# Optimization experiments

Measured on AMD Instinct MI355X. Metric: run time of the kernel, lower is better.

Reference implementation:

```python
import jax, jax.numpy as jnp
import numpy as np

B, N, D = 256, 131072, 256
TEMP = 0.05
EPS_SM = 1e-6
EPS_LOG = 1e-6
NUM_CLUSTERS = 1000


def _l2norm(x):
    return x / jnp.linalg.norm(x, axis=-1, keepdims=True)


def setup_inputs() -> dict:
    key = jax.random.key(0)
    k1, k2, k3, k4, k5 = jax.random.split(key, 5)
    # re-ID features are L2-normalized in practice; keeps exp(logits/temp) finite
    inputs = _l2norm(jax.random.normal(k1, (B, D), jnp.float32))
    indexes = jax.random.randint(k2, (B,), 0, N)
    labels = jax.random.randint(k3, (N,), 0, NUM_CLUSTERS)  # pseudo cluster ids buffer
    cluster_features = _l2norm(jax.random.normal(k4, (N, D), jnp.float32))
    instance_features = _l2norm(jax.random.normal(k5, (N, D), jnp.float32))
    return {
        "inputs": inputs,
        "cluster_features": cluster_features,
        "instance_features": instance_features,
        "indexes": indexes,
        "labels": labels,
    }


def reference(inputs, cluster_features, instance_features, indexes, labels):
    # targets = labels[indexes]
    targets = labels[indexes]
    # bank similarity GEMM, temperature scaling
    logits = jnp.matmul(inputs, cluster_features.T) / TEMP  # [B, N]
    # module's custom softmax: exp / (sum + eps)  (intentionally no max-subtract)
    exps = jnp.exp(logits)
    masked_sim = exps / (jnp.sum(exps, axis=1, keepdims=True) + EPS_SM)
    logp = jnp.log(masked_sim + EPS_LOG)
    # F.nll_loss: mean of -logp at target column
    loss = -jnp.mean(jnp.take_along_axis(logp, targets[:, None], axis=1))
    return loss
```

## Files before the change

kernel.cpp:

```cpp
#include <hip/hip_runtime.h>
#include <hip/hip_bf16.h>
#include <cstdint>

#define B_ 256
#define N_ 131072
#define D_ 256
#define INV_TEMP 20.0f
#define EPS_SM 1e-6f
#define EPS_LOG 1e-6f

#define TPB 512
#define BN 128
#define BK 64
#define TILES 4
#define LDB 72
#define BUFE (BN * LDB)
#define NSLOT 32

typedef __bf16 bf16_t;
typedef bf16_t bf16x8 __attribute__((ext_vector_type(8)));
typedef float f32x4 __attribute__((ext_vector_type(4)));

__device__ inline ushort f2bf(float f) {
  uint32_t u = __builtin_bit_cast(uint32_t, f);
  u += 0x7FFFu + ((u >> 16) & 1u);
  return (ushort)(u >> 16);
}

__global__ __launch_bounds__(TPB, 2)
void gemm_rowsum(const float* __restrict__ inp, const float* __restrict__ cf,
                 float* __restrict__ rowsum) {
  __shared__ ushort smem[2 * BUFE];
  const int tid  = threadIdx.x;
  const int wave = tid >> 6;
  const int lane = tid & 63;
  const int m15  = lane & 15;
  const int q    = lane >> 4;

  bf16x8 areg[8][2];
#pragma unroll
  for (int kc = 0; kc < 4; ++kc) {
    const int row = tid >> 1, half = tid & 1;
    const float* src = inp + row * D_ + kc * BK + half * 32;
#pragma unroll
    for (int i = 0; i < 8; ++i) {
      const float4 v = *(const float4*)(src + i * 4);
      ushort4 w = {f2bf(v.x), f2bf(v.y), f2bf(v.z), f2bf(v.w)};
      *(ushort4*)(&smem[row * LDB + half * 32 + i * 4]) = w;
    }
    __syncthreads();
#pragma unroll
    for (int mb = 0; mb < 2; ++mb)
#pragma unroll
      for (int ks = 0; ks < 2; ++ks)
        areg[kc * 2 + ks][mb] = __builtin_bit_cast(
            bf16x8, *(const uint4*)(&smem[(wave * 32 + mb * 16 + m15) * LDB + ks * 32 + q * 8]));
    __syncthreads();
  }

  const size_t nbase = (size_t)blockIdx.x * (TILES * BN);
  const int brow = tid >> 2, bcg = tid & 3;

  f32x4 acc[2][8];
  float rs[2][4];
#pragma unroll
  for (int mb = 0; mb < 2; ++mb) {
#pragma unroll
    for (int nb = 0; nb < 8; ++nb) acc[mb][nb] = (f32x4){0.f, 0.f, 0.f, 0.f};
#pragma unroll
    for (int r = 0; r < 4; ++r) rs[mb][r] = 0.f;
  }

  float4 ldbuf[2][4];
#define LDADDR(c) (cf + (nbase + (size_t)((c) >> 2) * BN + brow) * D_ + ((c) & 3) * BK + bcg * 16)

#pragma unroll
  for (int i = 0; i < 4; ++i) ldbuf[0][i] = *(const float4*)(LDADDR(0) + i * 4);
#pragma unroll
  for (int i = 0; i < 4; ++i) ldbuf[1][i] = *(const float4*)(LDADDR(1) + i * 4);
  {
    ushort* dst = &smem[0 * BUFE + brow * LDB + bcg * 16];
#pragma unroll
    for (int i = 0; i < 4; ++i) {
      const float4 v = ldbuf[0][i];
      ushort4 w = {f2bf(v.x), f2bf(v.y), f2bf(v.z), f2bf(v.w)};
      *(ushort4*)(dst + i * 4) = w;
    }
  }

#pragma unroll
  for (int c = 0; c < TILES * 4; ++c) {
    __syncthreads();
    if (c + 2 < TILES * 4) {
#pragma unroll
      for (int i = 0; i < 4; ++i) ldbuf[c & 1][i] = *(const float4*)(LDADDR(c + 2) + i * 4);
    }
    const ushort* bs = &smem[(c & 1) * BUFE];
#pragma unroll
    for (int ks = 0; ks < 2; ++ks) {
      bf16x8 bfr[8];
#pragma unroll
      for (int nb = 0; nb < 8; ++nb)
        bfr[nb] = __builtin_bit_cast(
            bf16x8, *(const uint4*)(&bs[(nb * 16 + m15) * LDB + ks * 32 + q * 8]));
#pragma unroll
      for (int mb = 0; mb < 2; ++mb)
#pragma unroll
        for (int nb = 0; nb < 8; ++nb)
          acc[mb][nb] = __builtin_amdgcn_mfma_f32_16x16x32_bf16(
              areg[(c & 3) * 2 + ks][mb], bfr[nb], acc[mb][nb], 0, 0, 0);
    }
    if ((c & 3) == 3) {
#pragma unroll
      for (int mb = 0; mb < 2; ++mb)
#pragma unroll
        for (int nb = 0; nb < 8; ++nb)
#pragma unroll
          for (int r = 0; r < 4; ++r)
            rs[mb][r] += __expf(acc[mb][nb][r] * INV_TEMP);
      if (c + 1 < TILES * 4) {
#pragma unroll
        for (int mb = 0; mb < 2; ++mb)
#pragma unroll
          for (int nb = 0; nb < 8; ++nb) acc[mb][nb] = (f32x4){0.f, 0.f, 0.f, 0.f};
      }
    }
    if (c + 1 < TILES * 4) {
      ushort* dst = &smem[((c + 1) & 1) * BUFE + brow * LDB + bcg * 16];
#pragma unroll
      for (int i = 0; i < 4; ++i) {
        const float4 v = ldbuf[(c + 1) & 1][i];
        ushort4 w = {f2bf(v.x), f2bf(v.y), f2bf(v.z), f2bf(v.w)};
        *(ushort4*)(dst + i * 4) = w;
      }
    }
  }

#pragma unroll
  for (int off = 8; off >= 1; off >>= 1)
#pragma unroll
    for (int mb = 0; mb < 2; ++mb)
#pragma unroll
      for (int r = 0; r < 4; ++r)
        rs[mb][r] += __shfl_xor(rs[mb][r], off, 64);

  if (m15 == 0) {
    float* slot = rowsum + (blockIdx.x & (NSLOT - 1)) * B_;
#pragma unroll
    for (int mb = 0; mb < 2; ++mb)
#pragma unroll
      for (int r = 0; r < 4; ++r)
        atomicAdd(&slot[wave * 32 + mb * 16 + q * 4 + r], rs[mb][r]);
  }
#undef LDADDR
}

__global__ __launch_bounds__(1024)
void finalize_loss(const float* __restrict__ inp, const float* __restrict__ cf,
                   const int* __restrict__ idx, const int* __restrict__ lab,
                   const float* __restrict__ rowsum, float* __restrict__ out) {
  __shared__ float red[1024];
  __shared__ float lg[256];
  const int tid = threadIdx.x;
  const int b = tid >> 2, part = tid & 3;
  const int t = lab[idx[b]];
  const float4* a = (const float4*)(inp + b * D_ + part * 64);
  const float4* c = (const float4*)(cf + (size_t)t * D_ + part * 64);
  float dot = 0.f;
#pragma unroll
  for (int i = 0; i < 16; ++i) {
    const float4 x = a[i], y = c[i];
    dot += x.x * y.x + x.y * y.y + x.z * y.z + x.w * y.w;
  }
  red[tid] = dot;
  __syncthreads();
  if (tid < 256) {
    const float d = red[tid * 4] + red[tid * 4 + 1] + red[tid * 4 + 2] + red[tid * 4 + 3];
    float S = 0.f;
#pragma unroll
    for (int s = 0; s < NSLOT; ++s) S += rowsum[s * B_ + tid];
    lg[tid] = __logf(__expf(d * INV_TEMP) / (S + EPS_SM) + EPS_LOG);
  }
  __syncthreads();
  for (int off = 128; off >= 1; off >>= 1) {
    if (tid < off) lg[tid] += lg[tid + off];
    __syncthreads();
  }
  if (tid == 0) out[0] = -lg[0] * (1.0f / 256.0f);
}

extern "C" void kernel_launch(void* const* d_in, const int* in_sizes, int n_in,
                              void* d_out, int out_size, void* d_ws, size_t ws_size,
                              hipStream_t stream) {
  const float* inp = (const float*)d_in[0];
  const float* cf  = (const float*)d_in[1];
  const int* idx = (const int*)d_in[3];
  const int* lab = (const int*)d_in[4];
  float* out = (float*)d_out;
  float* rowsum = (float*)d_ws;

  hipMemsetAsync(rowsum, 0, NSLOT * B_ * sizeof(float), stream);
  gemm_rowsum<<<dim3(N_ / (TILES * BN)), dim3(TPB), 0, stream>>>(inp, cf, rowsum);
  finalize_loss<<<dim3(1), dim3(1024), 0, stream>>>(inp, cf, idx, lab, rowsum, out);
}
```

Before: 287.8 us.

## Replace atomic rowsum slots with per-block partials and lighter LDS barrier

After: 290.8 us. No clear change (+1.1%).

```diff
diff --git a/kernel.cpp b/kernel.cpp
--- a/kernel.cpp
+++ b/kernel.cpp
@@ -13,9 +13,9 @@
 #define BN 128
 #define BK 64
 #define TILES 4
+#define NBLK (N_ / (TILES * BN))
 #define LDB 72
 #define BUFE (BN * LDB)
-#define NSLOT 32
 
 typedef __bf16 bf16_t;
 typedef bf16_t bf16x8 __attribute__((ext_vector_type(8)));
@@ -25,6 +25,10 @@
   uint32_t u = __builtin_bit_cast(uint32_t, f);
   u += 0x7FFFu + ((u >> 16) & 1u);
   return (ushort)(u >> 16);
+}
+
+__device__ inline void lds_barrier() {
+  asm volatile("s_waitcnt lgkmcnt(0)\n\ts_barrier" ::: "memory");
 }
 
 __global__ __launch_bounds__(TPB, 2)
@@ -90,7 +94,7 @@
 
 #pragma unroll
   for (int c = 0; c < TILES * 4; ++c) {
-    __syncthreads();
+    lds_barrier();
     if (c + 2 < TILES * 4) {
 #pragma unroll
       for (int i = 0; i < 4; ++i) ldbuf[c & 1][i] = *(const float4*)(LDADDR(c + 2) + i * 4);
@@ -145,12 +149,12 @@
         rs[mb][r] += __shfl_xor(rs[mb][r], off, 64);
 
   if (m15 == 0) {
-    float* slot = rowsum + (blockIdx.x & (NSLOT - 1)) * B_;
+    float* slot = rowsum + (size_t)blockIdx.x * B_;
 #pragma unroll
     for (int mb = 0; mb < 2; ++mb)
 #pragma unroll
       for (int r = 0; r < 4; ++r)
-        atomicAdd(&slot[wave * 32 + mb * 16 + q * 4 + r], rs[mb][r]);
+        slot[wave * 32 + mb * 16 + q * 4 + r] = rs[mb][r];
   }
 #undef LDADDR
 }
@@ -162,10 +166,11 @@
   __shared__ float red[1024];
   __shared__ float lg[256];
   const int tid = threadIdx.x;
-  const int b = tid >> 2, part = tid & 3;
-  const int t = lab[idx[b]];
-  const float4* a = (const float4*)(inp + b * D_ + part * 64);
-  const float4* c = (const float4*)(cf + (size_t)t * D_ + part * 64);
+  const int r = tid & 255, p = tid >> 8;
+
+  const int t = lab[idx[r]];
+  const float4* a = (const float4*)(inp + r * D_ + p * 64);
+  const float4* c = (const float4*)(cf + (size_t)t * D_ + p * 64);
   float dot = 0.f;
 #pragma unroll
   for (int i = 0; i < 16; ++i) {
@@ -173,13 +178,18 @@
     dot += x.x * y.x + x.y * y.y + x.z * y.z + x.w * y.w;
   }
   red[tid] = dot;
+
+  float S = 0.f;
+#pragma unroll 8
+  for (int j = 0; j < NBLK / 4; ++j) S += rowsum[(size_t)(p * (NBLK / 4) + j) * B_ + r];
+  __syncthreads();
+  const float d4 = red[r] + red[r + 256] + red[r + 512] + red[r + 768];
+  __syncthreads();
+  red[tid] = S;
   __syncthreads();
   if (tid < 256) {
-    const float d = red[tid * 4] + red[tid * 4 + 1] + red[tid * 4 + 2] + red[tid * 4 + 3];
-    float S = 0.f;
-#pragma unroll
-    for (int s = 0; s < NSLOT; ++s) S += rowsum[s * B_ + tid];
-    lg[tid] = __logf(__expf(d * INV_TEMP) / (S + EPS_SM) + EPS_LOG);
+    const float Sr = red[r] + red[r + 256] + red[r + 512] + red[r + 768];
+    lg[r] = __logf(__expf(d4 * INV_TEMP) / (Sr + EPS_SM) + EPS_LOG);
   }
   __syncthreads();
   for (int off = 128; off >= 1; off >>= 1) {
@@ -199,7 +209,6 @@
   float* out = (float*)d_out;
   float* rowsum = (float*)d_ws;
 
-  hipMemsetAsync(rowsum, 0, NSLOT * B_ * sizeof(float), stream);
-  gemm_rowsum<<<dim3(N_ / (TILES * BN)), dim3(TPB), 0, stream>>>(inp, cf, rowsum);
+  gemm_rowsum<<<dim3(NBLK), dim3(TPB), 0, stream>>>(inp, cf, rowsum);
   finalize_loss<<<dim3(1), dim3(1024), 0, stream>>>(inp, cf, idx, lab, rowsum, out);
 }
```
